# Optimization experiments

Hardware: AMD Instinct MI355X
Metric: run time of the kernel (lower is better)

The kernel has to match this reference:

```python
import jax, jax.numpy as jnp
import numpy as np

NUM_ITER = 3  # routing iterations (canonical CapsNet)
EPS = 1e-12


def _conv(x, w, stride):
    return jax.lax.conv_general_dilated(
        x, w, (stride, stride), 'VALID',
        dimension_numbers=('NCHW', 'OIHW', 'NCHW'))


def _squash(t, axis=-1):
    sn = (t * t).sum(axis=axis, keepdims=True)
    return sn / (1.0 + sn) * t / jnp.sqrt(sn + EPS)


def _batchnorm(x, eps=1e-5):
    # fresh BatchNorm2d in training mode: batch stats, weight=1, bias=0, biased var
    m = x.mean((0, 2, 3), keepdims=True)
    v = ((x - m) ** 2).mean((0, 2, 3), keepdims=True)
    return (x - m) * jax.lax.rsqrt(v + eps)


def _branch(x, cw, cb, pw, pb, rw):
    # x: [B,1,H,W]; cw: [128,1,k,k]; pw: [8,32,128,k,k]; rw: [10,R,8,16]
    y = jax.nn.relu(_conv(x, cw, 1) + cb[None, :, None, None])
    y = _batchnorm(y)
    nc, oc = pw.shape[0], pw.shape[1]  # 8 capsules, 32 channels each
    p = _conv(y, pw.reshape(nc * oc, pw.shape[2], pw.shape[3], pw.shape[4]), 2)
    p = p + pb.reshape(-1)[None, :, None, None]          # [B,256,h,w]
    B = p.shape[0]
    u = jnp.transpose(p.reshape(B, nc, -1), (0, 2, 1))   # [B,R,8], R=32*h*w
    u = _squash(u, axis=-1)
    priors = jnp.einsum('bri,nrio->nbro', u, rw)         # [10,B,R,16]
    b = jnp.zeros(priors.shape[:3] + (1,), priors.dtype)  # [10,B,R,1]
    for i in range(NUM_ITER):
        c = jax.nn.softmax(b, axis=2)                    # over route nodes
        v = _squash((c * priors).sum(axis=2, keepdims=True))  # [10,B,1,16]
        if i < NUM_ITER - 1:
            b = b + (priors * v).sum(axis=-1, keepdims=True)
    v = jnp.transpose(v[:, :, 0, :], (1, 0, 2))          # [B,10,16]
    return jnp.sqrt((v * v).sum(-1) + EPS)               # [B,10] capsule lengths


def setup_inputs() -> dict:
    key = jax.random.key(0)
    ks = jax.random.split(key, 16)
    s = 0.05
    return {
        'x': jax.random.normal(ks[0], (256, 1, 28, 28), jnp.float32),
        'conv1_w': jax.random.normal(ks[1], (128, 1, 3, 3), jnp.float32) * s,
        'conv1_b': jnp.zeros((128,), jnp.float32),
        'prim1_w': jax.random.normal(ks[2], (8, 32, 128, 3, 3), jnp.float32) * s,
        'prim1_b': jnp.zeros((8, 32), jnp.float32),
        'digit1_w': jax.random.normal(ks[3], (10, 128, 8, 16), jnp.float32),
        'conv2_w': jax.random.normal(ks[4], (128, 1, 5, 5), jnp.float32) * s,
        'conv2_b': jnp.zeros((128,), jnp.float32),
        'prim2_w': jax.random.normal(ks[5], (8, 32, 128, 5, 5), jnp.float32) * s,
        'prim2_b': jnp.zeros((8, 32), jnp.float32),
        'digit2_w': jax.random.normal(ks[6], (10, 288, 8, 16), jnp.float32),
        'conv3_w': jax.random.normal(ks[7], (128, 1, 9, 9), jnp.float32) * s,
        'conv3_b': jnp.zeros((128,), jnp.float32),
        'prim3_w': jax.random.normal(ks[8], (8, 32, 128, 9, 9), jnp.float32) * s,
        'prim3_b': jnp.zeros((8, 32), jnp.float32),
        'digit3_w': jax.random.normal(ks[9], (10, 1152, 8, 16), jnp.float32),
    }


def reference(x, conv1_w, conv1_b, prim1_w, prim1_b, digit1_w,
              conv2_w, conv2_b, prim2_w, prim2_b, digit2_w,
              conv3_w, conv3_b, prim3_w, prim3_b, digit3_w):
    img = x[:, 0]                                   # [B,28,28]
    B = img.shape[0]
    x3 = img                                        # 28x28
    x2 = img.reshape(B, 14, 2, 14, 2).mean((2, 4))  # 14x14 pyramid level
    x1 = x2.reshape(B, 7, 2, 7, 2).mean((2, 4))     # 7x7 pyramid level
    l1 = _branch(x1[:, None], conv1_w, conv1_b, prim1_w, prim1_b, digit1_w)
    l2 = _branch(x2[:, None], conv2_w, conv2_b, prim2_w, prim2_b, digit2_w)
    l3 = _branch(x3[:, None], conv3_w, conv3_b, prim3_w, prim3_b, digit3_w)
    return jax.nn.softmax(l1 + l2 + l3, axis=-1)    # [B,10]
```

## Files before the change

### kernel.cpp

```cpp
#include <hip/hip_runtime.h>
#include <math.h>

#define SQ_EPS 1e-12f
#define BN_EPS 1e-5f

typedef short short8 __attribute__((ext_vector_type(8)));
typedef float f32x4 __attribute__((ext_vector_type(4)));
typedef unsigned short ushort_t;

__device__ inline unsigned short f2bf(float x) {
    unsigned int u = __float_as_uint(x);
    unsigned int r = (u + 0x7fffu + ((u >> 16) & 1u)) >> 16;
    return (unsigned short)r;
}
__device__ inline float bf2f(unsigned short h) {
    return __uint_as_float(((unsigned int)h) << 16);
}

__device__ inline void gload_lds16(const ushort_t* g, ushort_t* l) {
    __builtin_amdgcn_global_load_lds(
        (const __attribute__((address_space(1))) void*)(g),
        (__attribute__((address_space(3))) void*)(l),
        16, 0, 0);
}

template<int IH, int IW, int KS, int OH, int OW>
__device__ void conv_body(const float* __restrict__ w, const float* __restrict__ bias,
                          ushort_t* __restrict__ yh, ushort_t* __restrict__ yl,
                          float* __restrict__ partial,
                          int b, int tid, float* s_img, float* s_w, float* s_red) {
    constexpr int KK = KS * KS;
    constexpr int OS = OH * OW;
    for (int i = tid; i < 128 * KK; i += 256) s_w[i] = w[i];
    __syncthreads();
    int c = tid & 127, half = tid >> 7;
    float bias_c = bias[c];
    float bsum = 0.f, bsq = 0.f;
    for (int r = half; r < OH; r += 2) {
        float acc[OW];
        #pragma unroll
        for (int j = 0; j < OW; ++j) acc[j] = bias_c;
        for (int u = 0; u < KS; ++u) {
            float rg[OW + KS - 1];
            #pragma unroll
            for (int j = 0; j < OW + KS - 1; ++j) rg[j] = s_img[(r + u) * IW + j];
            #pragma unroll
            for (int v = 0; v < KS; ++v) {
                float wv = s_w[c * KK + u * KS + v];
                #pragma unroll
                for (int j = 0; j < OW; ++j) acc[j] += wv * rg[j + v];
            }
        }
        #pragma unroll
        for (int j = 0; j < OW; ++j) {
            float val = fmaxf(acc[j], 0.f);
            bsum += val; bsq += val * val;
            unsigned short h = f2bf(val);
            unsigned short lo = f2bf(val - bf2f(h));
            int oidx = ((b * OS) + r * OW + j) * 128 + c;
            yh[oidx] = h; yl[oidx] = lo;
        }
    }
    s_red[tid] = bsum; __syncthreads();
    if (tid < 128) partial[b * 256 + c] = s_red[tid] + s_red[tid + 128];
    __syncthreads();
    s_red[tid] = bsq; __syncthreads();
    if (tid < 128) partial[b * 256 + 128 + c] = s_red[tid] + s_red[tid + 128];
}

__global__ __launch_bounds__(256) void conv_all_kernel(
        const float* __restrict__ img,
        const float* __restrict__ c1w, const float* __restrict__ c1b,
        const float* __restrict__ c2w, const float* __restrict__ c2b,
        const float* __restrict__ c3w, const float* __restrict__ c3b,
        ushort_t* __restrict__ yh1, ushort_t* __restrict__ yl1,
        ushort_t* __restrict__ yh2, ushort_t* __restrict__ yl2,
        ushort_t* __restrict__ yh3, ushort_t* __restrict__ yl3,
        float* __restrict__ partial_base) {
    __shared__ float s_img[784];
    __shared__ float s_tmp[196];
    __shared__ float s_w[128 * 81];
    __shared__ float s_red[256];
    int br = blockIdx.x >> 8, b = blockIdx.x & 255, tid = threadIdx.x;
    const float* im = img + b * 784;
    for (int i = tid; i < 784; i += 256) s_img[i] = im[i];
    __syncthreads();
    if (br <= 1) {
        for (int idx = tid; idx < 196; idx += 256) {
            int i = idx / 14, j = idx % 14;
            s_tmp[idx] = 0.25f * (s_img[(2*i)*28 + 2*j]   + s_img[(2*i)*28 + 2*j + 1] +
                                  s_img[(2*i+1)*28 + 2*j] + s_img[(2*i+1)*28 + 2*j + 1]);
        }
        __syncthreads();
        if (br == 0) {
            for (int idx = tid; idx < 49; idx += 256) {
                int i = idx / 7, j = idx % 7;
                s_img[idx] = 0.25f * (s_tmp[(2*i)*14 + 2*j]   + s_tmp[(2*i)*14 + 2*j + 1] +
                                      s_tmp[(2*i+1)*14 + 2*j] + s_tmp[(2*i+1)*14 + 2*j + 1]);
            }
        } else {
            for (int idx = tid; idx < 196; idx += 256) s_img[idx] = s_tmp[idx];
        }
        __syncthreads();
    }
    if (br == 0)      conv_body<7, 7, 3, 5, 5>(c1w, c1b, yh1, yl1, partial_base, b, tid, s_img, s_w, s_red);
    else if (br == 1) conv_body<14, 14, 5, 10, 10>(c2w, c2b, yh2, yl2, partial_base + 65536, b, tid, s_img, s_w, s_red);
    else              conv_body<28, 28, 9, 20, 20>(c3w, c3b, yh3, yl3, partial_base + 131072, b, tid, s_img, s_w, s_red);
}

__global__ void bn_final_kernel(const float* __restrict__ partial_base, float* __restrict__ bnp_base) {
    int br = blockIdx.x;
    const float* pp = partial_base + br * 65536;
    float* bnp = bnp_base + br * 512;
    float N = (br == 0) ? 6400.f : ((br == 1) ? 25600.f : 102400.f);
    int c = threadIdx.x;
    float s = 0.f, q = 0.f;
    for (int blk = 0; blk < 256; ++blk) {
        s += pp[blk * 256 + c];
        q += pp[blk * 256 + 128 + c];
    }
    float mean = s / N;
    float var = q / N - mean * mean;
    float inv = rsqrtf(var + BN_EPS);
    bnp[256 + c] = inv;
    bnp[384 + c] = -mean * inv;
}

__global__ __launch_bounds__(256) void wtrans_zero_kernel(
        const float* __restrict__ w1, const float* __restrict__ w2,
        const float* __restrict__ w3, const float* __restrict__ bnp_base,
        const float* __restrict__ pb1, const float* __restrict__ pb2,
        const float* __restrict__ pb3,
        ushort_t* __restrict__ wh1, ushort_t* __restrict__ wl1,
        ushort_t* __restrict__ wh2, ushort_t* __restrict__ wl2,
        ushort_t* __restrict__ wh3, ushort_t* __restrict__ wl3,
        float* __restrict__ b1, float* __restrict__ b2, float* __restrict__ b3,
        float* __restrict__ p3zero) {
    __shared__ float tile[128 * 81];
    __shared__ float r2[2];
    int blk = blockIdx.x, tid = threadIdx.x;
    if (blk >= 768) {
        ((float4*)p3zero)[(blk - 768) * 256 + tid] = (float4){0.f, 0.f, 0.f, 0.f};
        return;
    }
    int br = blk >> 8, ch = blk & 255;
    const float* w; const float* pb; ushort_t* wh; ushort_t* wl; float* bf; int KK;
    if (br == 0)      { w = w1; pb = pb1; wh = wh1; wl = wl1; bf = b1; KK = 9;  }
    else if (br == 1) { w = w2; pb = pb2; wh = wh2; wl = wl2; bf = b2; KK = 25; }
    else              { w = w3; pb = pb3; wh = wh3; wl = wl3; bf = b3; KK = 81; }
    const float* bnp = bnp_base + br * 512;
    int n = 128 * KK;
    const float* wrow = w + ch * n;
    for (int i = tid; i < n; i += 256) tile[i] = wrow[i];
    __syncthreads();
    for (int j = tid; j < n; j += 256) {
        int uv = j >> 7, c = j & 127;
        float val = tile[c * KK + uv] * bnp[256 + c];
        unsigned short h = f2bf(val);
        unsigned short lo = f2bf(val - bf2f(h));
        int oidx = uv * 32768 + (ch << 7) + c;
        wh[oidx] = h; wl[oidx] = lo;
    }
    float s = 0.f;
    if (tid < 128) {
        for (int uv = 0; uv < KK; ++uv) s += tile[tid * KK + uv];
        s *= bnp[384 + tid];
    }
    for (int off = 32; off; off >>= 1) s += __shfl_down(s, off);
    if (tid < 128 && (tid & 63) == 0) r2[tid >> 6] = s;
    __syncthreads();
    if (tid == 0) bf[ch] = pb[ch] + r2[0] + r2[1];
}

template<int S, int WO, int IHg, int IWg, int KS, int ZCH>
__device__ void gemm_body(const ushort_t* __restrict__ yh, const ushort_t* __restrict__ yl,
                          const ushort_t* __restrict__ wh, const ushort_t* __restrict__ wl,
                          float* __restrict__ p, int bx, int by, int bz, int tid,
                          ushort_t* Ash, ushort_t* Asl, ushort_t* Bsh, ushort_t* Bsl) {
    int bm = bx * 128, ch0 = by * 128;
    int arow = tid >> 2;
    int c0 = tid & 3;
    int c0s = c0 ^ ((arow >> 1) & 3);
    int lane = tid & 63, wid = tid >> 6;
    int wb0 = wid * 512;
    int wb1 = 64 * 32 + wid * 512;
    int m0 = bm + arow;
    int b0 = m0 / S, s0 = m0 % S;
    int abase0 = ((b0 * IHg + 2 * (s0 / WO)) * IWg + 2 * (s0 % WO)) * 128 + c0s * 8;
    int m1 = m0 + 64;
    int b1 = m1 / S, s1 = m1 % S;
    int abase1 = ((b1 * IHg + 2 * (s1 / WO)) * IWg + 2 * (s1 % WO)) * 128 + c0s * 8;
    int bbase0 = (ch0 + arow) * 128 + c0s * 8;
    int bbase1 = (ch0 + arow + 64) * 128 + c0s * 8;
    int wm = (tid >> 6) & 1, wn = tid >> 7;
    int quad = lane >> 4, l16 = lane & 15;
    int aoffL[4], boffL[4];
    #pragma unroll
    for (int mi = 0; mi < 4; ++mi) {
        int row = wm * 64 + mi * 16 + l16;
        aoffL[mi] = row * 32 + ((quad ^ ((row >> 1) & 3)) * 8);
    }
    #pragma unroll
    for (int ni = 0; ni < 4; ++ni) {
        int row = wn * 64 + ni * 16 + l16;
        boffL[ni] = row * 32 + ((quad ^ ((row >> 1) & 3)) * 8);
    }
    f32x4 acc[4][4];
    #pragma unroll
    for (int mi = 0; mi < 4; ++mi)
        #pragma unroll
        for (int ni = 0; ni < 4; ++ni)
            acc[mi][ni] = (f32x4){0.f, 0.f, 0.f, 0.f};

    int kc = bz * ZCH;
    int uv = kc >> 2, ci = kc & 3;
    int u = uv / KS, v = uv - u * KS;
    int aoff = (u * IWg + v) * 128 + (ci << 5);
    int boff = uv * 32768 + (ci << 5);

    #define GEMM_ADV() do { ci = (ci + 1) & 3;                                   \
        if (ci == 0) { ++uv; ++v; if (v == KS) { v = 0; ++u; } }                 \
        aoff = (u * IWg + v) * 128 + (ci << 5);                                  \
        boff = uv * 32768 + (ci << 5); } while (0)
    #define GEMM_ISSUE(BSEL) do { int o_ = (BSEL) * 4096;                        \
        gload_lds16(yh + abase0 + aoff, Ash + o_ + wb0);                         \
        gload_lds16(yl + abase0 + aoff, Asl + o_ + wb0);                         \
        gload_lds16(yh + abase1 + aoff, Ash + o_ + wb1);                         \
        gload_lds16(yl + abase1 + aoff, Asl + o_ + wb1);                         \
        gload_lds16(wh + bbase0 + boff, Bsh + o_ + wb0);                         \
        gload_lds16(wl + bbase0 + boff, Bsl + o_ + wb0);                         \
        gload_lds16(wh + bbase1 + boff, Bsh + o_ + wb1);                         \
        gload_lds16(wl + bbase1 + boff, Bsl + o_ + wb1); } while (0)

    GEMM_ISSUE(0); GEMM_ADV();
    GEMM_ISSUE(1); GEMM_ADV();

    for (int t = 0; t < ZCH; ++t) {
        if (t < ZCH - 1) { asm volatile("s_waitcnt vmcnt(8)" ::: "memory"); }
        else             { asm volatile("s_waitcnt vmcnt(0)" ::: "memory"); }
        asm volatile("s_barrier" ::: "memory");
        int bo = (t & 1) * 4096;
        short8 bh[4], bl[4];
        #pragma unroll
        for (int ni = 0; ni < 4; ++ni) {
            bh[ni] = *reinterpret_cast<const short8*>(&Bsh[bo + boffL[ni]]);
            bl[ni] = *reinterpret_cast<const short8*>(&Bsl[bo + boffL[ni]]);
        }
        #pragma unroll
        for (int mi = 0; mi < 4; ++mi) {
            short8 ah = *reinterpret_cast<const short8*>(&Ash[bo + aoffL[mi]]);
            short8 al = *reinterpret_cast<const short8*>(&Asl[bo + aoffL[mi]]);
            #pragma unroll
            for (int ni = 0; ni < 4; ++ni) {
                acc[mi][ni] = __builtin_amdgcn_mfma_f32_16x16x32_bf16(ah, bh[ni], acc[mi][ni], 0, 0, 0);
                acc[mi][ni] = __builtin_amdgcn_mfma_f32_16x16x32_bf16(al, bh[ni], acc[mi][ni], 0, 0, 0);
                acc[mi][ni] = __builtin_amdgcn_mfma_f32_16x16x32_bf16(ah, bl[ni], acc[mi][ni], 0, 0, 0);
            }
        }
        asm volatile("s_barrier" ::: "memory");
        if (t + 3 <= ZCH) {
            GEMM_ISSUE(t & 1);
            GEMM_ADV();
        }
    }
    #undef GEMM_ISSUE
    #undef GEMM_ADV

    #pragma unroll
    for (int mi = 0; mi < 4; ++mi)
        #pragma unroll
        for (int ni = 0; ni < 4; ++ni) {
            int col = ch0 + wn * 64 + ni * 16 + l16;
            #pragma unroll
            for (int reg = 0; reg < 4; ++reg) {
                int row = bm + wm * 64 + mi * 16 + quad * 4 + reg;
                atomicAdd(p + (size_t)row * 256 + col, acc[mi][ni][reg]);
            }
        }
}

__global__ __launch_bounds__(256, 2) void gemm3_kernel(
        const ushort_t* __restrict__ yh, const ushort_t* __restrict__ yl,
        const ushort_t* __restrict__ wh, const ushort_t* __restrict__ wl,
        float* __restrict__ p) {
    __shared__ ushort_t Ash[2 * 4096], Asl[2 * 4096];
    __shared__ ushort_t Bsh[2 * 4096], Bsl[2 * 4096];
    int bid = blockIdx.x + 72 * (blockIdx.y + 2 * blockIdx.z);
    int swz = (bid & 7) * 108 + (bid >> 3);
    int x = swz % 72, r = swz / 72;
    gemm_body<36, 6, 20, 20, 9, 54>(yh, yl, wh, wl, p,
                                    x, r & 1, r >> 1, threadIdx.x,
                                    Ash, Asl, Bsh, Bsl);
}

__global__ __launch_bounds__(256, 2) void gemm21_kernel(
        const ushort_t* __restrict__ yh2, const ushort_t* __restrict__ yl2,
        const ushort_t* __restrict__ wh2, const ushort_t* __restrict__ wl2, float* __restrict__ p2,
        const ushort_t* __restrict__ yh1, const ushort_t* __restrict__ yl1,
        const ushort_t* __restrict__ wh1, const ushort_t* __restrict__ wl1, float* __restrict__ p1) {
    __shared__ ushort_t Ash[2 * 4096], Asl[2 * 4096];
    __shared__ ushort_t Bsh[2 * 4096], Bsl[2 * 4096];
    int bid = blockIdx.x;
    int swz = (bid & 7) * 63 + (bid >> 3);
    int tid = threadIdx.x;
    if (swz < 360) {
        int z = swz / 36, rem = swz % 36, y = rem / 18, x = rem % 18;
        gemm_body<9, 3, 10, 10, 5, 10>(yh2, yl2, wh2, wl2, p2, x, y, z, tid, Ash, Asl, Bsh, Bsl);
    } else {
        int b = swz - 360;
        int z = b / 16, rem = b % 16, y = rem / 8, x = rem % 8;
        gemm_body<4, 2, 5, 5, 3, 4>(yh1, yl1, wh1, wl1, p1, x, y, z, tid, Ash, Asl, Bsh, Bsl);
    }
}

__global__ void squash_all_kernel(const float* __restrict__ p1, const float* __restrict__ p2,
                                  const float* __restrict__ p3,
                                  const float* __restrict__ bias1, const float* __restrict__ bias2,
                                  const float* __restrict__ bias3,
                                  float* __restrict__ u1, float* __restrict__ u2,
                                  float* __restrict__ u3) {
    int blk = blockIdx.x;
    const float* p; const float* bias; float* u; int S;
    if (blk < 128)      { p = p1; bias = bias1; u = u1; S = 4; }
    else if (blk < 416) { p = p2; bias = bias2; u = u2; S = 9;  blk -= 128; }
    else                { p = p3; bias = bias3; u = u3; S = 36; blk -= 416; }
    int idx = blk * 256 + threadIdx.x;
    int o = idx & 31, rest = idx >> 5;
    int s = rest % S, b = rest / S;
    const float* pp = p + (size_t)(b * S + s) * 256 + o;
    float t[8]; float sn = 0.f;
    #pragma unroll
    for (int i = 0; i < 8; ++i) { t[i] = pp[i * 32] + bias[o + i * 32]; sn += t[i] * t[i]; }
    float f = sn / ((1.f + sn) * sqrtf(sn + SQ_EPS));
    float* up = u + (size_t)(b * (32 * S) + o * S + s) * 8;
    float4 w0 = {t[0] * f, t[1] * f, t[2] * f, t[3] * f};
    float4 w1 = {t[4] * f, t[5] * f, t[6] * f, t[7] * f};
    *reinterpret_cast<float4*>(up) = w0;
    *reinterpret_cast<float4*>(up + 4) = w1;
}

__global__ void rwtrans_zero_kernel(const float* __restrict__ w1, const float* __restrict__ w2,
                                    const float* __restrict__ w3,
                                    float* __restrict__ o1, float* __restrict__ o2,
                                    float* __restrict__ o3,
                                    float* __restrict__ p2, float* __restrict__ p1) {
    int blk = blockIdx.x;
    if (blk >= 7840) {
        int zb = blk - 7840;
        if (zb < 576) ((float4*)p2)[zb * 256 + threadIdx.x] = (float4){0.f, 0.f, 0.f, 0.f};
        else          ((float4*)p1)[(zb - 576) * 256 + threadIdx.x] = (float4){0.f, 0.f, 0.f, 0.f};
        return;
    }
    int idx = blk * 256 + threadIdx.x;
    if (idx < 163840) {
        int t = idx;
        int jj = t & 3; t >>= 2;
        int r = t & 127; t >>= 7;
        int g2 = t & 31; int n = t >> 5;
        o1[idx] = w1[(n * 128 + r) * 128 + g2 * 4 + jj];
    } else if (idx < 532480) {
        int t = idx - 163840;
        int jj = t & 3; t >>= 2;
        int r = t % 288; t /= 288;
        int g2 = t & 31; int n = t >> 5;
        o2[idx - 163840] = w2[(n * 288 + r) * 128 + g2 * 4 + jj];
    } else {
        int t = idx - 532480;
        int jj = t & 3; t >>= 2;
        int r = t % 1152; t /= 1152;
        int g2 = t & 31; int n = t >> 5;
        o3[idx - 532480] = w3[(n * 1152 + r) * 128 + g2 * 4 + jj];
    }
}

template<int R>
__device__ void routing_body(const float* __restrict__ u, const float* __restrict__ rwt,
                             float* __restrict__ lens, int n, int b, int tid,
                             float* red, float* vsh, float* sred) {
    constexpr int KMAX = (R + 255) / 256;
    constexpr float invR = 1.0f / (float)R;
    int lane = tid & 63, wv = tid >> 6;

    unsigned int d[KMAX][8];
    float a[16];
    float blog[KMAX];
    float v[16];

    #pragma unroll
    for (int o = 0; o < 16; ++o) a[o] = 0.f;
    #pragma unroll
    for (int k = 0; k < KMAX; ++k) blog[k] = 0.f;

    #pragma unroll
    for (int k = 0; k < KMAX; ++k) {
        int r = tid + k * 256;
        if (r < R) {
            const float4* up = (const float4*)(u + ((size_t)b * R + r) * 8);
            float4 ua = up[0], ub2 = up[1];
            float uu[8] = {ua.x, ua.y, ua.z, ua.w, ub2.x, ub2.y, ub2.z, ub2.w};
            float po[16];
            #pragma unroll
            for (int o = 0; o < 16; ++o) po[o] = 0.f;
            #pragma unroll
            for (int g2 = 0; g2 < 32; ++g2) {
                float4 w4 = *reinterpret_cast<const float4*>(rwt + (((size_t)n * 32 + g2) * R + r) * 4);
                float ui = uu[g2 >> 2];
                int o0 = (g2 & 3) * 4;
                po[o0 + 0] += ui * w4.x;
                po[o0 + 1] += ui * w4.y;
                po[o0 + 2] += ui * w4.z;
                po[o0 + 3] += ui * w4.w;
            }
            #pragma unroll
            for (int j = 0; j < 8; ++j)
                d[k][j] = (unsigned int)f2bf(po[2*j]) | ((unsigned int)f2bf(po[2*j+1]) << 16);
            #pragma unroll
            for (int o = 0; o < 16; ++o) a[o] += po[o];
        }
    }

    for (int it = 0; it < 3; ++it) {
        if (it > 0) {
            float lsum = 0.f;
            #pragma unroll
            for (int o = 0; o < 16; ++o) a[o] = 0.f;
            #pragma unroll
            for (int k = 0; k < KMAX; ++k) {
                int r = tid + k * 256;
                if (r < R) {
                    float pv[16];
                    #pragma unroll
                    for (int j = 0; j < 8; ++j) {
                        pv[2*j]   = __uint_as_float(d[k][j] << 16);
                        pv[2*j+1] = __uint_as_float(d[k][j] & 0xffff0000u);
                    }
                    float dt0 = 0.f, dt1 = 0.f, dt2 = 0.f, dt3 = 0.f;
                    #pragma unroll
                    for (int o = 0; o < 4; ++o) {
                        dt0 += pv[o]      * v[o];
                        dt1 += pv[4 + o]  * v[4 + o];
                        dt2 += pv[8 + o]  * v[8 + o];
                        dt3 += pv[12 + o] * v[12 + o];
                    }
                    blog[k] += (dt0 + dt1) + (dt2 + dt3);
                    float e = __expf(blog[k]);
                    lsum += e;
                    #pragma unroll
                    for (int o = 0; o < 16; ++o) a[o] += e * pv[o];
                }
            }
            lsum += __shfl_xor(lsum, 1);
            lsum += __shfl_xor(lsum, 2);
            lsum += __shfl_xor(lsum, 4);
            lsum += __shfl_xor(lsum, 8);
            lsum += __shfl_xor(lsum, 16);
            lsum += __shfl_xor(lsum, 32);
            if (lane == 0) sred[wv] = lsum;
        }
        #pragma unroll
        for (int k2 = 0; k2 < 4; ++k2) {
            int m = 1 << k2;
            int lb = (lane >> k2) & 1;
            #pragma unroll
            for (int t = 0; t < (8 >> k2); ++t) {
                float x0 = a[2 * t], x1 = a[2 * t + 1];
                float keep = lb ? x1 : x0;
                float send = lb ? x0 : x1;
                a[t] = keep + __shfl_xor(send, m);
            }
        }
        float tot = a[0];
        tot += __shfl_xor(tot, 16);
        tot += __shfl_xor(tot, 32);
        if (lane < 16) red[wv * 16 + lane] = tot;
        __syncthreads();
        if (tid < 16) {
            float vo = red[tid] + red[16 + tid] + red[32 + tid] + red[48 + tid];
            float scale = (it == 0) ? invR
                                    : 1.0f / (sred[0] + sred[1] + sred[2] + sred[3]);
            vo *= scale;
            float sn = vo * vo;
            sn += __shfl_xor(sn, 1);
            sn += __shfl_xor(sn, 2);
            sn += __shfl_xor(sn, 4);
            sn += __shfl_xor(sn, 8);
            float f = sn / ((1.f + sn) * sqrtf(sn + SQ_EPS));
            if (it == 2) {
                if (tid == 0) lens[b * 10 + n] = sqrtf(sn * f * f + SQ_EPS);
            } else {
                vsh[tid] = vo * f;
            }
        }
        __syncthreads();
        if (it < 2) {
            #pragma unroll
            for (int o = 0; o < 16; ++o) v[o] = vsh[o];
        }
    }
}

__global__ __launch_bounds__(256, 2) void routing_all_kernel(
        const float* __restrict__ u1, const float* __restrict__ u2, const float* __restrict__ u3,
        const float* __restrict__ rwt1, const float* __restrict__ rwt2,
        const float* __restrict__ rwt3,
        float* __restrict__ l1, float* __restrict__ l2, float* __restrict__ l3) {
    __shared__ float red[64];
    __shared__ float vsh[16];
    __shared__ float sred[4];
    int n = blockIdx.x, b = blockIdx.y, br = 2 - blockIdx.z, tid = threadIdx.x;
    if (br == 0)      routing_body<128>(u1, rwt1, l1, n, b, tid, red, vsh, sred);
    else if (br == 1) routing_body<288>(u2, rwt2, l2, n, b, tid, red, vsh, sred);
    else              routing_body<1152>(u3, rwt3, l3, n, b, tid, red, vsh, sred);
}

__global__ void final_softmax_kernel(const float* __restrict__ l1, const float* __restrict__ l2,
                                     const float* __restrict__ l3, float* __restrict__ out) {
    int b = threadIdx.x;
    float v[10]; float mx = -1e30f;
    #pragma unroll
    for (int n = 0; n < 10; ++n) {
        v[n] = l1[b * 10 + n] + l2[b * 10 + n] + l3[b * 10 + n];
        mx = fmaxf(mx, v[n]);
    }
    float s = 0.f;
    #pragma unroll
    for (int n = 0; n < 10; ++n) { v[n] = expf(v[n] - mx); s += v[n]; }
    float inv = 1.f / s;
    #pragma unroll
    for (int n = 0; n < 10; ++n) out[b * 10 + n] = v[n] * inv;
}

extern "C" void kernel_launch(void* const* d_in, const int* in_sizes, int n_in,
                              void* d_out, int out_size, void* d_ws, size_t ws_size,
                              hipStream_t stream) {
    const float* x   = (const float*)d_in[0];
    const float* c1w = (const float*)d_in[1];
    const float* c1b = (const float*)d_in[2];
    const float* p1w = (const float*)d_in[3];
    const float* p1b = (const float*)d_in[4];
    const float* d1w = (const float*)d_in[5];
    const float* c2w = (const float*)d_in[6];
    const float* c2b = (const float*)d_in[7];
    const float* p2w = (const float*)d_in[8];
    const float* p2b = (const float*)d_in[9];
    const float* d2w = (const float*)d_in[10];
    const float* c3w = (const float*)d_in[11];
    const float* c3b = (const float*)d_in[12];
    const float* p3w = (const float*)d_in[13];
    const float* p3b = (const float*)d_in[14];
    const float* d3w = (const float*)d_in[15];

    float* ws = (float*)d_ws;
    float* yh1f  = ws + 62720;
    float* yl1f  = ws + 472320;
    float* yh2f  = ws + 881920;
    float* yl2f  = ws + 2520320;
    float* yh3f  = ws + 4158720;
    float* yl3f  = ws + 10712320;
    float* wh1f  = ws + 17265920;
    float* wl1f  = ws + 17413376;
    float* wh2f  = ws + 17560832;
    float* wl2f  = ws + 17970432;
    float* wh3f  = ws + 18380032;
    float* wl3f  = ws + 19707136;
    float* p3    = ws + 21034240;
    float* bnp1  = ws + 23393536;
    float* bias1 = ws + 23395072;
    float* bias2 = ws + 23395328;
    float* bias3 = ws + 23395584;
    float* l1    = ws + 23395840;
    float* l2    = ws + 23398400;
    float* l3    = ws + 23400960;

    ushort_t* yh1 = (ushort_t*)yh1f; ushort_t* yl1 = (ushort_t*)yl1f;
    ushort_t* yh2 = (ushort_t*)yh2f; ushort_t* yl2 = (ushort_t*)yl2f;
    ushort_t* yh3 = (ushort_t*)yh3f; ushort_t* yl3 = (ushort_t*)yl3f;
    ushort_t* wh1 = (ushort_t*)wh1f; ushort_t* wl1 = (ushort_t*)wl1f;
    ushort_t* wh2 = (ushort_t*)wh2f; ushort_t* wl2 = (ushort_t*)wl2f;
    ushort_t* wh3 = (ushort_t*)wh3f; ushort_t* wl3 = (ushort_t*)wl3f;
    float* u1 = yh1f;
    float* u2 = yh2f;
    float* u3 = yh3f;
    float* p2 = wh3f;
    float* p1 = wl3f;
    float* rwt1 = yl3f;
    float* rwt2 = rwt1 + 163840;
    float* rwt3 = rwt2 + 368640;

    conv_all_kernel<<<768, 256, 0, stream>>>(x, c1w, c1b, c2w, c2b, c3w, c3b,
                                             yh1, yl1, yh2, yl2, yh3, yl3, p3);
    bn_final_kernel<<<3, 128, 0, stream>>>(p3, bnp1);
    wtrans_zero_kernel<<<3072, 256, 0, stream>>>(p1w, p2w, p3w, bnp1, p1b, p2b, p3b,
                                                 wh1, wl1, wh2, wl2, wh3, wl3,
                                                 bias1, bias2, bias3, p3);
    gemm3_kernel<<<dim3(72, 2, 6), 256, 0, stream>>>(yh3, yl3, wh3, wl3, p3);
    rwtrans_zero_kernel<<<8672, 256, 0, stream>>>(d1w, d2w, d3w, rwt1, rwt2, rwt3, p2, p1);
    gemm21_kernel<<<504, 256, 0, stream>>>(yh2, yl2, wh2, wl2, p2, yh1, yl1, wh1, wl1, p1);
    squash_all_kernel<<<1568, 256, 0, stream>>>(p1, p2, p3, bias1, bias2, bias3, u1, u2, u3);
    routing_all_kernel<<<dim3(10, 256, 3), 256, 0, stream>>>(u1, u2, u3, rwt1, rwt2, rwt3, l1, l2, l3);
    final_softmax_kernel<<<1, 256, 0, stream>>>(l1, l2, l3, (float*)d_out);
}
```

Baseline: 494.7 us.

## Load GEMM operands directly from global into registers, dropping LDS staging

The primary-capsule GEMM no longer stages A/B tiles through shared memory with global_load_lds and barriers. Each lane now loads its MFMA fragments straight from global memory into registers, double-buffered across two k-steps. This removes LDS traffic and the per-step barriers. In exchange, operands shared across waves are fetched redundantly from global/L2 (each wave reloads A and B), register pressure rises, and the 16-byte loads per lane are strided rather than coalesced.

```diff
diff --git a/kernel.cpp b/kernel.cpp
--- a/kernel.cpp
+++ b/kernel.cpp
@@ -15,13 +15,6 @@
 }
 __device__ inline float bf2f(unsigned short h) {
     return __uint_as_float(((unsigned int)h) << 16);
-}
-
-__device__ inline void gload_lds16(const ushort_t* g, ushort_t* l) {
-    __builtin_amdgcn_global_load_lds(
-        (const __attribute__((address_space(1))) void*)(g),
-        (__attribute__((address_space(3))) void*)(l),
-        16, 0, 0);
 }
 
 template<int IH, int IW, int KS, int OH, int OW>
@@ -175,36 +168,24 @@
 template<int S, int WO, int IHg, int IWg, int KS, int ZCH>
 __device__ void gemm_body(const ushort_t* __restrict__ yh, const ushort_t* __restrict__ yl,
                           const ushort_t* __restrict__ wh, const ushort_t* __restrict__ wl,
-                          float* __restrict__ p, int bx, int by, int bz, int tid,
-                          ushort_t* Ash, ushort_t* Asl, ushort_t* Bsh, ushort_t* Bsl) {
+                          float* __restrict__ p, int bx, int by, int bz, int tid) {
+    static_assert((ZCH & 1) == 0, "2-step unroll needs even ZCH");
     int bm = bx * 128, ch0 = by * 128;
-    int arow = tid >> 2;
-    int c0 = tid & 3;
-    int c0s = c0 ^ ((arow >> 1) & 3);
     int lane = tid & 63, wid = tid >> 6;
-    int wb0 = wid * 512;
-    int wb1 = 64 * 32 + wid * 512;
-    int m0 = bm + arow;
-    int b0 = m0 / S, s0 = m0 % S;
-    int abase0 = ((b0 * IHg + 2 * (s0 / WO)) * IWg + 2 * (s0 % WO)) * 128 + c0s * 8;
-    int m1 = m0 + 64;
-    int b1 = m1 / S, s1 = m1 % S;
-    int abase1 = ((b1 * IHg + 2 * (s1 / WO)) * IWg + 2 * (s1 % WO)) * 128 + c0s * 8;
-    int bbase0 = (ch0 + arow) * 128 + c0s * 8;
-    int bbase1 = (ch0 + arow + 64) * 128 + c0s * 8;
-    int wm = (tid >> 6) & 1, wn = tid >> 7;
+    int wm = wid & 1, wn = wid >> 1;
     int quad = lane >> 4, l16 = lane & 15;
-    int aoffL[4], boffL[4];
+    int q8 = quad * 8;
+    int abaseL[4], bbaseL[4];
     #pragma unroll
     for (int mi = 0; mi < 4; ++mi) {
-        int row = wm * 64 + mi * 16 + l16;
-        aoffL[mi] = row * 32 + ((quad ^ ((row >> 1) & 3)) * 8);
-    }
-    #pragma unroll
-    for (int ni = 0; ni < 4; ++ni) {
-        int row = wn * 64 + ni * 16 + l16;
-        boffL[ni] = row * 32 + ((quad ^ ((row >> 1) & 3)) * 8);
-    }
+        int m = bm + wm * 64 + mi * 16 + l16;
+        int b = m / S, s = m % S;
+        abaseL[mi] = ((b * IHg + 2 * (s / WO)) * IWg + 2 * (s % WO)) * 128 + q8;
+    }
+    #pragma unroll
+    for (int ni = 0; ni < 4; ++ni)
+        bbaseL[ni] = (ch0 + wn * 64 + ni * 16 + l16) * 128 + q8;
+
     f32x4 acc[4][4];
     #pragma unroll
     for (int mi = 0; mi < 4; ++mi)
@@ -222,49 +203,44 @@
         if (ci == 0) { ++uv; ++v; if (v == KS) { v = 0; ++u; } }                 \
         aoff = (u * IWg + v) * 128 + (ci << 5);                                  \
         boff = uv * 32768 + (ci << 5); } while (0)
-    #define GEMM_ISSUE(BSEL) do { int o_ = (BSEL) * 4096;                        \
-        gload_lds16(yh + abase0 + aoff, Ash + o_ + wb0);                         \
-        gload_lds16(yl + abase0 + aoff, Asl + o_ + wb0);                         \
-        gload_lds16(yh + abase1 + aoff, Ash + o_ + wb1);                         \
-        gload_lds16(yl + abase1 + aoff, Asl + o_ + wb1);                         \
-        gload_lds16(wh + bbase0 + boff, Bsh + o_ + wb0);                         \
-        gload_lds16(wl + bbase0 + boff, Bsl + o_ + wb0);                         \
-        gload_lds16(wh + bbase1 + boff, Bsh + o_ + wb1);                         \
-        gload_lds16(wl + bbase1 + boff, Bsl + o_ + wb1); } while (0)
-
-    GEMM_ISSUE(0); GEMM_ADV();
-    GEMM_ISSUE(1); GEMM_ADV();
-
-    for (int t = 0; t < ZCH; ++t) {
-        if (t < ZCH - 1) { asm volatile("s_waitcnt vmcnt(8)" ::: "memory"); }
-        else             { asm volatile("s_waitcnt vmcnt(0)" ::: "memory"); }
-        asm volatile("s_barrier" ::: "memory");
-        int bo = (t & 1) * 4096;
-        short8 bh[4], bl[4];
-        #pragma unroll
-        for (int ni = 0; ni < 4; ++ni) {
-            bh[ni] = *reinterpret_cast<const short8*>(&Bsh[bo + boffL[ni]]);
-            bl[ni] = *reinterpret_cast<const short8*>(&Bsl[bo + boffL[ni]]);
-        }
-        #pragma unroll
-        for (int mi = 0; mi < 4; ++mi) {
-            short8 ah = *reinterpret_cast<const short8*>(&Ash[bo + aoffL[mi]]);
-            short8 al = *reinterpret_cast<const short8*>(&Asl[bo + aoffL[mi]]);
-            #pragma unroll
-            for (int ni = 0; ni < 4; ++ni) {
-                acc[mi][ni] = __builtin_amdgcn_mfma_f32_16x16x32_bf16(ah, bh[ni], acc[mi][ni], 0, 0, 0);
-                acc[mi][ni] = __builtin_amdgcn_mfma_f32_16x16x32_bf16(al, bh[ni], acc[mi][ni], 0, 0, 0);
-                acc[mi][ni] = __builtin_amdgcn_mfma_f32_16x16x32_bf16(ah, bl[ni], acc[mi][ni], 0, 0, 0);
-            }
-        }
-        asm volatile("s_barrier" ::: "memory");
-        if (t + 3 <= ZCH) {
-            GEMM_ISSUE(t & 1);
-            GEMM_ADV();
-        }
-    }
-    #undef GEMM_ISSUE
+    #define LOADSET(AH, AL, BH, BL) do {                                         \
+        _Pragma("unroll")                                                        \
+        for (int mi = 0; mi < 4; ++mi) {                                         \
+            AH[mi] = *reinterpret_cast<const short8*>(yh + abaseL[mi] + aoff);   \
+            AL[mi] = *reinterpret_cast<const short8*>(yl + abaseL[mi] + aoff);   \
+        }                                                                        \
+        _Pragma("unroll")                                                        \
+        for (int ni = 0; ni < 4; ++ni) {                                         \
+            BH[ni] = *reinterpret_cast<const short8*>(wh + bbaseL[ni] + boff);   \
+            BL[ni] = *reinterpret_cast<const short8*>(wl + bbaseL[ni] + boff);   \
+        }                                                                        \
+    } while (0)
+    #define MFMA_BLK(AH, AL, BH, BL) do {                                        \
+        _Pragma("unroll")                                                        \
+        for (int mi = 0; mi < 4; ++mi) {                                         \
+            _Pragma("unroll")                                                    \
+            for (int ni = 0; ni < 4; ++ni) {                                     \
+                acc[mi][ni] = __builtin_amdgcn_mfma_f32_16x16x32_bf16(AH[mi], BH[ni], acc[mi][ni], 0, 0, 0); \
+                acc[mi][ni] = __builtin_amdgcn_mfma_f32_16x16x32_bf16(AL[mi], BH[ni], acc[mi][ni], 0, 0, 0); \
+                acc[mi][ni] = __builtin_amdgcn_mfma_f32_16x16x32_bf16(AH[mi], BL[ni], acc[mi][ni], 0, 0, 0); \
+            }                                                                    \
+        }                                                                        \
+    } while (0)
+
+    short8 Ah0[4], Al0[4], Bh0[4], Bl0[4];
+    short8 Ah1[4], Al1[4], Bh1[4], Bl1[4];
+    LOADSET(Ah0, Al0, Bh0, Bl0); GEMM_ADV();
+    LOADSET(Ah1, Al1, Bh1, Bl1); GEMM_ADV();
+
+    for (int t = 0; t < ZCH; t += 2) {
+        MFMA_BLK(Ah0, Al0, Bh0, Bl0);
+        if (t + 2 < ZCH) { LOADSET(Ah0, Al0, Bh0, Bl0); GEMM_ADV(); }
+        MFMA_BLK(Ah1, Al1, Bh1, Bl1);
+        if (t + 3 < ZCH) { LOADSET(Ah1, Al1, Bh1, Bl1); GEMM_ADV(); }
+    }
     #undef GEMM_ADV
+    #undef LOADSET
+    #undef MFMA_BLK
 
     #pragma unroll
     for (int mi = 0; mi < 4; ++mi)
@@ -283,14 +259,11 @@
         const ushort_t* __restrict__ yh, const ushort_t* __restrict__ yl,
         const ushort_t* __restrict__ wh, const ushort_t* __restrict__ wl,
         float* __restrict__ p) {
-    __shared__ ushort_t Ash[2 * 4096], Asl[2 * 4096];
-    __shared__ ushort_t Bsh[2 * 4096], Bsl[2 * 4096];
     int bid = blockIdx.x + 72 * (blockIdx.y + 2 * blockIdx.z);
     int swz = (bid & 7) * 108 + (bid >> 3);
     int x = swz % 72, r = swz / 72;
     gemm_body<36, 6, 20, 20, 9, 54>(yh, yl, wh, wl, p,
-                                    x, r & 1, r >> 1, threadIdx.x,
-                                    Ash, Asl, Bsh, Bsl);
+                                    x, r & 1, r >> 1, threadIdx.x);
 }
 
 __global__ __launch_bounds__(256, 2) void gemm21_kernel(
@@ -298,18 +271,16 @@
         const ushort_t* __restrict__ wh2, const ushort_t* __restrict__ wl2, float* __restrict__ p2,
         const ushort_t* __restrict__ yh1, const ushort_t* __restrict__ yl1,
         const ushort_t* __restrict__ wh1, const ushort_t* __restrict__ wl1, float* __restrict__ p1) {
-    __shared__ ushort_t Ash[2 * 4096], Asl[2 * 4096];
-    __shared__ ushort_t Bsh[2 * 4096], Bsl[2 * 4096];
     int bid = blockIdx.x;
     int swz = (bid & 7) * 63 + (bid >> 3);
     int tid = threadIdx.x;
     if (swz < 360) {
         int z = swz / 36, rem = swz % 36, y = rem / 18, x = rem % 18;
-        gemm_body<9, 3, 10, 10, 5, 10>(yh2, yl2, wh2, wl2, p2, x, y, z, tid, Ash, Asl, Bsh, Bsl);
+        gemm_body<9, 3, 10, 10, 5, 10>(yh2, yl2, wh2, wl2, p2, x, y, z, tid);
     } else {
         int b = swz - 360;
         int z = b / 16, rem = b % 16, y = rem / 8, x = rem % 8;
-        gemm_body<4, 2, 5, 5, 3, 4>(yh1, yl1, wh1, wl1, p1, x, y, z, tid, Ash, Asl, Bsh, Bsl);
+        gemm_body<4, 2, 5, 5, 3, 4>(yh1, yl1, wh1, wl1, p1, x, y, z, tid);
     }
 }
 
```

New measurement: 748.3 us. +51.3%, slower.
